# Kernel optimization log

Hardware: AMD Instinct MI355X
Metric: run time of the kernel (lower is better)

Reference implementation:

```python
import jax, jax.numpy as jnp
import numpy as np

B, N, C, H = 8, 1024, 1024, 16
HD = C // H
SCALE = HD ** -0.5


def setup_inputs() -> dict:
    key = jax.random.key(0)
    ks = jax.random.split(key, 6)
    s = 0.02
    return {
        "x": jax.random.normal(ks[0], (B, N, C), dtype=jnp.float32),
        "z_cls": jax.random.normal(ks[1], (B, 2 * C), dtype=jnp.float32),
        "Wqkv": jax.random.normal(ks[2], (C, 3 * C), dtype=jnp.float32) * s,
        "Wkv_cls": jax.random.normal(ks[3], (2 * C, 2 * C), dtype=jnp.float32) * s,
        "Wproj": jax.random.normal(ks[4], (C, C), dtype=jnp.float32) * s,
        "bproj": jax.random.normal(ks[5], (C,), dtype=jnp.float32) * s,
    }


def reference(x, z_cls, Wqkv, Wkv_cls, Wproj, bproj):
    # qkv projection: [B,N,3C] -> q,k,v each [B,H,N,HD]
    qkv = (x @ Wqkv).reshape(B, N, 3, H, HD).transpose(2, 0, 3, 1, 4)
    q, k, v = qkv[0], qkv[1], qkv[2]
    # cls k/v: [B,2C] -> [B,H,1,HD] each
    kv_cls = (z_cls @ Wkv_cls).reshape(B, 1, 2, H, HD).transpose(2, 0, 3, 1, 4)
    k_cls, v_cls = kv_cls[0], kv_cls[1]
    k = jnp.concatenate([k_cls, k], axis=2)  # [B,H,N+1,HD]
    v = jnp.concatenate([v_cls, v], axis=2)
    attn = jax.nn.softmax(jnp.einsum("bhnd,bhmd->bhnm", q, k) * SCALE, axis=-1)
    out = jnp.einsum("bhnm,bhmd->bhnd", attn, v)  # [B,H,N,HD]
    out = out.transpose(0, 2, 1, 3).reshape(B, N, C)
    return out @ Wproj + bproj
```

## Files before the change

kernel.cpp:

```cpp
#include <hip/hip_runtime.h>


typedef __attribute__((ext_vector_type(8))) short bf16x8;
typedef __attribute__((ext_vector_type(8))) unsigned short u16x8;
typedef __attribute__((ext_vector_type(4))) float f32x4;

#define SL2E 0.18033688011112042f

__device__ __forceinline__ unsigned short f2bf(float f) {
  unsigned int u = __builtin_bit_cast(unsigned int, f);
  return (unsigned short)((u + 0x7FFFu + ((u >> 16) & 1u)) >> 16);
}

__device__ __forceinline__ unsigned int cvt_pk_bf16(float lo, float hi) {
  unsigned int r;
  asm("v_cvt_pk_bf16_f32 %0, %1, %2" : "=v"(r) : "v"(lo), "v"(hi));
  return r;
}

template <typename T>
__device__ __forceinline__ void gll16(const T* g, void* l) {
  __builtin_amdgcn_global_load_lds(
      (__attribute__((address_space(1))) void*)(const_cast<T*>(g)),
      (__attribute__((address_space(3))) void*)l, 16, 0, 0);
}

__global__ __launch_bounds__(256) void cvt_f2b(const float* __restrict__ in,
                                               unsigned short* __restrict__ out, int n) {
  int i = (blockIdx.x * 256 + threadIdx.x) * 8;
  if (i >= n) return;
  const float4* p4 = (const float4*)(in + i);
  float4 a = p4[0], b = p4[1];
  u16x8 o;
  o[0] = f2bf(a.x); o[1] = f2bf(a.y); o[2] = f2bf(a.z); o[3] = f2bf(a.w);
  o[4] = f2bf(b.x); o[5] = f2bf(b.y); o[6] = f2bf(b.z); o[7] = f2bf(b.w);
  *(u16x8*)(out + i) = o;
}

__global__ __launch_bounds__(256) void transpose_f2b(const float* __restrict__ in,
                                                     unsigned short* __restrict__ out,
                                                     int R, int C) {
  __shared__ float tile[32][33];
  int c0 = blockIdx.x * 32, r0 = blockIdx.y * 32;
  int tx = threadIdx.x, ty = threadIdx.y;
#pragma unroll
  for (int j = 0; j < 32; j += 8)
    tile[ty + j][tx] = in[(size_t)(r0 + ty + j) * C + c0 + tx];
  __syncthreads();
#pragma unroll
  for (int j = 0; j < 32; j += 8)
    out[(size_t)(c0 + ty + j) * R + r0 + tx] = f2bf(tile[tx][ty + j]);
}

__global__ __launch_bounds__(256) void kvcls_gemm(const float* __restrict__ z,
                                                  const float* __restrict__ W,
                                                  float* __restrict__ accum) {
  int cc = blockIdx.x >> 5;
  int kc = blockIdx.x & 31;
  int c = cc * 256 + threadIdx.x;
  int k0 = kc * 64;
  float acc[8] = {0, 0, 0, 0, 0, 0, 0, 0};
  const float* wp = W + (size_t)k0 * 2048 + c;
  for (int k = 0; k < 64; ++k) {
    float wv = wp[(size_t)k * 2048];
#pragma unroll
    for (int b = 0; b < 8; ++b) acc[b] += z[b * 2048 + k0 + k] * wv;
  }
#pragma unroll
  for (int b = 0; b < 8; ++b) atomicAdd(&accum[b * 2048 + c], acc[b]);
}

__global__ __launch_bounds__(256) void kvcls_scatter(const float* __restrict__ accum,
                                                     unsigned short* __restrict__ kbuf,
                                                     unsigned short* __restrict__ vbuf) {
  int i = blockIdx.x * 256 + threadIdx.x;
  int b = i >> 11, c = i & 2047;
  int t = c >> 10, h = (c >> 6) & 15, d = c & 63;
  int bh = b * 16 + h;
  unsigned short v = f2bf(accum[i]);
  if (t == 0) kbuf[((size_t)bh * 1088 + 0) * 64 + d] = v;
  else        vbuf[((size_t)bh * 64 + d) * 1088 + 0] = v;
}

__global__ __launch_bounds__(256) void gemm_qkv(const unsigned short* __restrict__ A,
                                                const unsigned short* __restrict__ Bt,
                                                unsigned short* __restrict__ qb,
                                                unsigned short* __restrict__ kbuf,
                                                unsigned short* __restrict__ vbuf) {
  constexpr int K = 1024;
  __shared__ __attribute__((aligned(16))) unsigned short As[128 * 64];
  __shared__ __attribute__((aligned(16))) unsigned short Bs[128 * 64];
  int t = threadIdx.x, w = t >> 6, l = t & 63;
  int wg = (blockIdx.x & 7) * 192 + (blockIdx.x >> 3);
  int tm = wg / 24, tn = wg % 24;
  int m0 = tm * 128, n0 = tn * 128;
  int wr = w >> 1, wc = w & 1;
  int g = l >> 4, q = l & 15;
  f32x4 acc[4][4] = {};
  for (int kt = 0; kt < K / 64; ++kt) {
    int k0 = kt * 64;
#pragma unroll
    for (int i = 0; i < 4; ++i) {
      int f = i * 4096 + t * 16;
      int row = f >> 7, colb = (f & 127) ^ ((row & 7) << 4);
      gll16(A + (size_t)(m0 + row) * K + k0 + (colb >> 1), (char*)As + f);
    }
#pragma unroll
    for (int i = 0; i < 4; ++i) {
      int f = i * 4096 + t * 16;
      int row = f >> 7, colb = (f & 127) ^ ((row & 7) << 4);
      gll16(Bt + (size_t)(n0 + row) * K + k0 + (colb >> 1), (char*)Bs + f);
    }
    __syncthreads();
#pragma unroll
    for (int kk = 0; kk < 2; ++kk) {
      bf16x8 af[4], bf[4];
#pragma unroll
      for (int m = 0; m < 4; ++m) {
        int row = wr * 64 + m * 16 + q;
        int cb = (kk * 64 + g * 16) ^ ((row & 7) << 4);
        af[m] = *(const bf16x8*)((const char*)As + row * 128 + cb);
      }
#pragma unroll
      for (int n = 0; n < 4; ++n) {
        int row = wc * 64 + n * 16 + q;
        int cb = (kk * 64 + g * 16) ^ ((row & 7) << 4);
        bf[n] = *(const bf16x8*)((const char*)Bs + row * 128 + cb);
      }
      __builtin_amdgcn_s_setprio(1);
#pragma unroll
      for (int m = 0; m < 4; ++m)
#pragma unroll
        for (int n = 0; n < 4; ++n)
          acc[m][n] = __builtin_amdgcn_mfma_f32_16x16x32_bf16(af[m], bf[n], acc[m][n], 0, 0, 0);
      __builtin_amdgcn_s_setprio(0);
    }
    __syncthreads();
  }
  int tsel = n0 >> 10;
  int b = m0 >> 10;
  int nqb = m0 & 1023, ncb = n0 & 1023;
#pragma unroll
  for (int m = 0; m < 4; ++m)
#pragma unroll
    for (int n = 0; n < 4; ++n)
#pragma unroll
      for (int r = 0; r < 4; ++r) {
        int nq = nqb + wr * 64 + m * 16 + g * 4 + r;
        int col = ncb + wc * 64 + n * 16 + q;
        int h = col >> 6, d = col & 63;
        int bh = b * 16 + h;
        unsigned short val = f2bf(acc[m][n][r]);
        if (tsel == 0)      qb[((size_t)bh * 1024 + nq) * 64 + d] = val;
        else if (tsel == 1) kbuf[((size_t)bh * 1088 + 1 + nq) * 64 + d] = val;
        else                vbuf[((size_t)bh * 64 + d) * 1088 + 1 + nq] = val;
      }
}

__global__ __launch_bounds__(256) void attn_kernel(const unsigned short* __restrict__ qbuf,
                                                   const unsigned short* __restrict__ kbuf,
                                                   const unsigned short* __restrict__ vbuf,
                                                   unsigned short* __restrict__ ob) {
  __shared__ __attribute__((aligned(16))) unsigned short Ks[2][64 * 64];
  __shared__ __attribute__((aligned(16))) unsigned short Vs[2][64 * 64];
  __shared__ __attribute__((aligned(16))) unsigned short Ps[4][16 * 64];
  int t = threadIdx.x, w = t >> 6, l = t & 63;
  int g = l >> 4, q = l & 15;
  int wg = (blockIdx.x & 7) * 256 + (blockIdx.x >> 3);
  int bh = wg >> 4, qt = wg & 15;

  const unsigned short* qrow = qbuf + ((size_t)bh * 1024 + qt * 64 + w * 16 + q) * 64;
  bf16x8 qf[2];
  qf[0] = *(const bf16x8*)(qrow + g * 8);
  qf[1] = *(const bf16x8*)(qrow + 32 + g * 8);

  const unsigned short* kg = kbuf + (size_t)bh * 1088 * 64;
  const unsigned short* vg = vbuf + (size_t)bh * 64 * 1088;
  char* Pw = (char*)Ps[w];

  auto STAGE = [&](int bb, int kt) {
#pragma unroll
    for (int i = 0; i < 2; ++i) {
      int f = i * 4096 + t * 16;
      int row = f >> 7, colb = (f & 127) ^ ((row & 7) << 4);
      gll16(kg + (size_t)(kt * 64 + row) * 64 + (colb >> 1), (char*)Ks[bb] + f);
      gll16(vg + (size_t)row * 1088 + kt * 64 + (colb >> 1), (char*)Vs[bb] + f);
    }
  };

  STAGE(0, 0);
  __syncthreads();

  f32x4 o[4] = {};
  float mrun = -__builtin_inff(), lrun = 0.f;
  int swz = (q & 7) << 4;

  for (int kt = 0; kt < 17; ++kt) {
    int cur = kt & 1;
    if (kt < 16) STAGE(cur ^ 1, kt + 1);
    f32x4 s[4] = {};
#pragma unroll
    for (int kk = 0; kk < 2; ++kk) {
      bf16x8 kf[4];
#pragma unroll
      for (int n = 0; n < 4; ++n) {
        int cb = (kk * 64 + g * 16) ^ swz;
        kf[n] = *(const bf16x8*)((const char*)Ks[cur] + (n * 16 + q) * 128 + cb);
      }
      __builtin_amdgcn_s_setprio(1);
#pragma unroll
      for (int n = 0; n < 4; ++n)
        s[n] = __builtin_amdgcn_mfma_f32_16x16x32_bf16(kf[n], qf[kk], s[n], 0, 0, 0);
      __builtin_amdgcn_s_setprio(0);
    }
    if (kt == 16) {
#pragma unroll
      for (int n = 0; n < 4; ++n)
#pragma unroll
        for (int r = 0; r < 4; ++r)
          if (n | r) s[n][r] = -__builtin_inff();
      if (g != 0) s[0][0] = -__builtin_inff();
    }
    float mx = fmaxf(fmaxf(fmaxf(s[0][0], s[0][1]), fmaxf(s[0][2], s[0][3])),
                     fmaxf(fmaxf(s[1][0], s[1][1]), fmaxf(s[1][2], s[1][3])));
    mx = fmaxf(mx, fmaxf(fmaxf(fmaxf(s[2][0], s[2][1]), fmaxf(s[2][2], s[2][3])),
                         fmaxf(fmaxf(s[3][0], s[3][1]), fmaxf(s[3][2], s[3][3]))));
    mx = fmaxf(mx, __shfl_xor(mx, 16));
    mx = fmaxf(mx, __shfl_xor(mx, 32));
    float mnew;
    if (__all(mx <= mrun + 64.f)) {
      mnew = mrun;
    } else {
      mnew = fmaxf(mrun, mx);
      float fc = exp2f((mrun - mnew) * SL2E);
      mrun = mnew;
      lrun *= fc;
#pragma unroll
      for (int n = 0; n < 4; ++n) {
        o[n][0] *= fc; o[n][1] *= fc; o[n][2] *= fc; o[n][3] *= fc;
      }
    }
    float nb = mnew * SL2E;
    float rs = 0.f;
#pragma unroll
    for (int n = 0; n < 4; ++n)
#pragma unroll
      for (int r = 0; r < 4; ++r) {
        float p = exp2f(s[n][r] * SL2E - nb);
        s[n][r] = p;
        rs += p;
      }
    rs += __shfl_xor(rs, 16);
    rs += __shfl_xor(rs, 32);
    lrun += rs;
#pragma unroll
    for (int n = 0; n < 4; ++n) {
      uint2 pk;
      pk.x = cvt_pk_bf16(s[n][0], s[n][1]);
      pk.y = cvt_pk_bf16(s[n][2], s[n][3]);
      *(uint2*)(Pw + q * 128 + ((n * 32 + g * 8) ^ swz)) = pk;
    }
    asm volatile("s_waitcnt lgkmcnt(0)" ::: "memory");
#pragma unroll
    for (int kk = 0; kk < 2; ++kk) {
      bf16x8 pb = *(const bf16x8*)(Pw + q * 128 + ((kk * 64 + g * 16) ^ swz));
      bf16x8 vf[4];
#pragma unroll
      for (int n = 0; n < 4; ++n) {
        int cb = (kk * 64 + g * 16) ^ swz;
        vf[n] = *(const bf16x8*)((const char*)Vs[cur] + (n * 16 + q) * 128 + cb);
      }
      __builtin_amdgcn_s_setprio(1);
#pragma unroll
      for (int n = 0; n < 4; ++n)
        o[n] = __builtin_amdgcn_mfma_f32_16x16x32_bf16(vf[n], pb, o[n], 0, 0, 0);
      __builtin_amdgcn_s_setprio(0);
    }
    __syncthreads();
  }
  int b = bh >> 4, h = bh & 15;
  float inv = 1.0f / lrun;
  size_t rowg = (size_t)b * 1024 + qt * 64 + w * 16 + q;
#pragma unroll
  for (int n = 0; n < 4; ++n) {
    uint2 pk;
    pk.x = cvt_pk_bf16(o[n][0] * inv, o[n][1] * inv);
    pk.y = cvt_pk_bf16(o[n][2] * inv, o[n][3] * inv);
    *(uint2*)(ob + rowg * 1024 + h * 64 + n * 16 + g * 4) = pk;
  }
}

__global__ __launch_bounds__(256) void gemm_proj(const unsigned short* __restrict__ A,
                                                 const unsigned short* __restrict__ Bt,
                                                 const float* __restrict__ bias,
                                                 float* __restrict__ out) {
  constexpr int K = 1024;
  __shared__ __attribute__((aligned(16))) unsigned short As[128 * 64];
  __shared__ __attribute__((aligned(16))) unsigned short Bs[128 * 64];
  int t = threadIdx.x, w = t >> 6, l = t & 63;
  int wg = (blockIdx.x & 7) * 64 + (blockIdx.x >> 3);
  int tm = wg / 8, tn = wg % 8;
  int m0 = tm * 128, n0 = tn * 128;
  int wr = w >> 1, wc = w & 1;
  int g = l >> 4, q = l & 15;
  f32x4 acc[4][4] = {};
  for (int kt = 0; kt < K / 64; ++kt) {
    int k0 = kt * 64;
#pragma unroll
    for (int i = 0; i < 4; ++i) {
      int f = i * 4096 + t * 16;
      int row = f >> 7, colb = (f & 127) ^ ((row & 7) << 4);
      gll16(A + (size_t)(m0 + row) * K + k0 + (colb >> 1), (char*)As + f);
    }
#pragma unroll
    for (int i = 0; i < 4; ++i) {
      int f = i * 4096 + t * 16;
      int row = f >> 7, colb = (f & 127) ^ ((row & 7) << 4);
      gll16(Bt + (size_t)(n0 + row) * K + k0 + (colb >> 1), (char*)Bs + f);
    }
    __syncthreads();
#pragma unroll
    for (int kk = 0; kk < 2; ++kk) {
      bf16x8 af[4], bf[4];
#pragma unroll
      for (int m = 0; m < 4; ++m) {
        int row = wr * 64 + m * 16 + q;
        int cb = (kk * 64 + g * 16) ^ ((row & 7) << 4);
        af[m] = *(const bf16x8*)((const char*)As + row * 128 + cb);
      }
#pragma unroll
      for (int n = 0; n < 4; ++n) {
        int row = wc * 64 + n * 16 + q;
        int cb = (kk * 64 + g * 16) ^ ((row & 7) << 4);
        bf[n] = *(const bf16x8*)((const char*)Bs + row * 128 + cb);
      }
      __builtin_amdgcn_s_setprio(1);
#pragma unroll
      for (int m = 0; m < 4; ++m)
#pragma unroll
        for (int n = 0; n < 4; ++n)
          acc[m][n] = __builtin_amdgcn_mfma_f32_16x16x32_bf16(af[m], bf[n], acc[m][n], 0, 0, 0);
      __builtin_amdgcn_s_setprio(0);
    }
    __syncthreads();
  }
  float bv[4];
#pragma unroll
  for (int n = 0; n < 4; ++n) bv[n] = bias[n0 + wc * 64 + n * 16 + q];
#pragma unroll
  for (int m = 0; m < 4; ++m)
#pragma unroll
    for (int r = 0; r < 4; ++r) {
      size_t row = m0 + wr * 64 + m * 16 + g * 4 + r;
#pragma unroll
      for (int n = 0; n < 4; ++n) {
        int col = n0 + wc * 64 + n * 16 + q;
        out[row * 1024 + col] = acc[m][n][r] + bv[n];
      }
    }
}

extern "C" void kernel_launch(void* const* d_in, const int* in_sizes, int n_in,
                              void* d_out, int out_size, void* d_ws, size_t ws_size,
                              hipStream_t stream) {
  const float* x       = (const float*)d_in[0];
  const float* z_cls   = (const float*)d_in[1];
  const float* Wqkv    = (const float*)d_in[2];
  const float* Wkv_cls = (const float*)d_in[3];
  const float* Wproj   = (const float*)d_in[4];
  const float* bproj   = (const float*)d_in[5];
  float* out = (float*)d_out;

  char* p = (char*)d_ws;
  unsigned short* x_bf    = (unsigned short*)p; p += (size_t)8192 * 1024 * 2;
  unsigned short* wqkv_t  = (unsigned short*)p; p += (size_t)3072 * 1024 * 2;
  unsigned short* wproj_t = (unsigned short*)p; p += (size_t)1024 * 1024 * 2;
  unsigned short* q_buf   = (unsigned short*)p; p += (size_t)128 * 1024 * 64 * 2;
  unsigned short* k_buf   = (unsigned short*)p; p += (size_t)128 * 1088 * 64 * 2;
  unsigned short* v_buf   = (unsigned short*)p; p += (size_t)128 * 64 * 1088 * 2;
  unsigned short* attn_o  = (unsigned short*)p; p += (size_t)8192 * 1024 * 2;
  float* accum            = (float*)p;          p += (size_t)8 * 2048 * 4;

  hipMemsetAsync(accum, 0, 8 * 2048 * 4, stream);
  cvt_f2b<<<4096, 256, 0, stream>>>(x, x_bf, 8388608);
  transpose_f2b<<<dim3(96, 32), dim3(32, 8), 0, stream>>>(Wqkv, wqkv_t, 1024, 3072);
  transpose_f2b<<<dim3(32, 32), dim3(32, 8), 0, stream>>>(Wproj, wproj_t, 1024, 1024);
  kvcls_gemm<<<256, 256, 0, stream>>>(z_cls, Wkv_cls, accum);
  kvcls_scatter<<<64, 256, 0, stream>>>(accum, k_buf, v_buf);
  gemm_qkv<<<1536, 256, 0, stream>>>(x_bf, wqkv_t, q_buf, k_buf, v_buf);
  attn_kernel<<<2048, 256, 0, stream>>>(q_buf, k_buf, v_buf, attn_o);
  gemm_proj<<<512, 256, 0, stream>>>(attn_o, wproj_t, bproj, out);
}
```

Measured before the change: 319.3 us.

## Double-buffer QKV and projection GEMMs with larger 256-row tiles and 512 threads

Both GEMMs now use larger block tiles (256x256 for QKV, 256x128 for projection) with 8 waves per block. A double-buffered LDS pipeline prefetches the next K-slice via global_load_lds while the current one is consumed, synchronised with vmcnt waits and raw barriers. This aims to hide global-load latency and raise data reuse per LDS byte. In exchange it uses more LDS and registers per block, and on 256 CUs the grids of 384 and 256 blocks fill the machine less evenly.

```diff
diff --git a/kernel.cpp b/kernel.cpp
--- a/kernel.cpp
+++ b/kernel.cpp
@@ -82,71 +82,84 @@
   else        vbuf[((size_t)bh * 64 + d) * 1088 + 0] = v;
 }
 
-__global__ __launch_bounds__(256) void gemm_qkv(const unsigned short* __restrict__ A,
-                                                const unsigned short* __restrict__ Bt,
-                                                unsigned short* __restrict__ qb,
-                                                unsigned short* __restrict__ kbuf,
-                                                unsigned short* __restrict__ vbuf) {
-  constexpr int K = 1024;
-  __shared__ __attribute__((aligned(16))) unsigned short As[128 * 64];
-  __shared__ __attribute__((aligned(16))) unsigned short Bs[128 * 64];
+__global__ __launch_bounds__(512, 2) void gemm_qkv(const unsigned short* __restrict__ A,
+                                                   const unsigned short* __restrict__ Bt,
+                                                   unsigned short* __restrict__ qb,
+                                                   unsigned short* __restrict__ kbuf,
+                                                   unsigned short* __restrict__ vbuf) {
+  __shared__ __attribute__((aligned(16))) unsigned short As[2][256 * 64];
+  __shared__ __attribute__((aligned(16))) unsigned short Bs[2][256 * 64];
   int t = threadIdx.x, w = t >> 6, l = t & 63;
-  int wg = (blockIdx.x & 7) * 192 + (blockIdx.x >> 3);
-  int tm = wg / 24, tn = wg % 24;
-  int m0 = tm * 128, n0 = tn * 128;
-  int wr = w >> 1, wc = w & 1;
   int g = l >> 4, q = l & 15;
-  f32x4 acc[4][4] = {};
-  for (int kt = 0; kt < K / 64; ++kt) {
-    int k0 = kt * 64;
+  int wg = ((int)blockIdx.x & 7) * 48 + ((int)blockIdx.x >> 3);
+  int tm = wg / 12, tn = wg % 12;
+  int m0 = tm * 256, n0 = tn * 256;
+  int wr = w >> 2, wc = w & 3;
+
+  auto STAGE = [&](int bb, int k0) {
 #pragma unroll
     for (int i = 0; i < 4; ++i) {
-      int f = i * 4096 + t * 16;
+      int f = i * 8192 + t * 16;
       int row = f >> 7, colb = (f & 127) ^ ((row & 7) << 4);
-      gll16(A + (size_t)(m0 + row) * K + k0 + (colb >> 1), (char*)As + f);
+      gll16(A + (size_t)(m0 + row) * 1024 + k0 + (colb >> 1), (char*)As[bb] + f);
     }
 #pragma unroll
     for (int i = 0; i < 4; ++i) {
-      int f = i * 4096 + t * 16;
+      int f = i * 8192 + t * 16;
       int row = f >> 7, colb = (f & 127) ^ ((row & 7) << 4);
-      gll16(Bt + (size_t)(n0 + row) * K + k0 + (colb >> 1), (char*)Bs + f);
-    }
-    __syncthreads();
+      gll16(Bt + (size_t)(n0 + row) * 1024 + k0 + (colb >> 1), (char*)Bs[bb] + f);
+    }
+  };
+
+  f32x4 acc[8][4] = {};
+  STAGE(0, 0);
+  for (int kt = 0; kt < 16; ++kt) {
+    int cur = kt & 1;
+    if (kt < 15) {
+      STAGE(cur ^ 1, (kt + 1) * 64);
+      asm volatile("s_waitcnt vmcnt(8)" ::: "memory");
+    } else {
+      asm volatile("s_waitcnt vmcnt(0)" ::: "memory");
+    }
+    __builtin_amdgcn_s_barrier();
+    asm volatile("" ::: "memory");
+    const char* Ac = (const char*)As[cur];
+    const char* Bc = (const char*)Bs[cur];
 #pragma unroll
     for (int kk = 0; kk < 2; ++kk) {
-      bf16x8 af[4], bf[4];
-#pragma unroll
-      for (int m = 0; m < 4; ++m) {
-        int row = wr * 64 + m * 16 + q;
-        int cb = (kk * 64 + g * 16) ^ ((row & 7) << 4);
-        af[m] = *(const bf16x8*)((const char*)As + row * 128 + cb);
+      bf16x8 af[8], bf[4];
+#pragma unroll
+      for (int m = 0; m < 8; ++m) {
+        int row = wr * 128 + m * 16 + q;
+        af[m] = *(const bf16x8*)(Ac + row * 128 + ((kk * 64 + g * 16) ^ ((row & 7) << 4)));
       }
 #pragma unroll
       for (int n = 0; n < 4; ++n) {
         int row = wc * 64 + n * 16 + q;
-        int cb = (kk * 64 + g * 16) ^ ((row & 7) << 4);
-        bf[n] = *(const bf16x8*)((const char*)Bs + row * 128 + cb);
+        bf[n] = *(const bf16x8*)(Bc + row * 128 + ((kk * 64 + g * 16) ^ ((row & 7) << 4)));
       }
       __builtin_amdgcn_s_setprio(1);
 #pragma unroll
-      for (int m = 0; m < 4; ++m)
+      for (int m = 0; m < 8; ++m)
 #pragma unroll
         for (int n = 0; n < 4; ++n)
           acc[m][n] = __builtin_amdgcn_mfma_f32_16x16x32_bf16(af[m], bf[n], acc[m][n], 0, 0, 0);
       __builtin_amdgcn_s_setprio(0);
     }
-    __syncthreads();
+    asm volatile("" ::: "memory");
+    __builtin_amdgcn_s_barrier();
+    asm volatile("" ::: "memory");
   }
   int tsel = n0 >> 10;
   int b = m0 >> 10;
   int nqb = m0 & 1023, ncb = n0 & 1023;
 #pragma unroll
-  for (int m = 0; m < 4; ++m)
+  for (int m = 0; m < 8; ++m)
 #pragma unroll
     for (int n = 0; n < 4; ++n)
 #pragma unroll
       for (int r = 0; r < 4; ++r) {
-        int nq = nqb + wr * 64 + m * 16 + g * 4 + r;
+        int nq = nqb + wr * 128 + m * 16 + g * 4 + r;
         int col = ncb + wc * 64 + n * 16 + q;
         int h = col >> 6, d = col & 63;
         int bh = b * 16 + h;
@@ -290,71 +303,84 @@
   }
 }
 
-__global__ __launch_bounds__(256) void gemm_proj(const unsigned short* __restrict__ A,
-                                                 const unsigned short* __restrict__ Bt,
-                                                 const float* __restrict__ bias,
-                                                 float* __restrict__ out) {
-  constexpr int K = 1024;
-  __shared__ __attribute__((aligned(16))) unsigned short As[128 * 64];
-  __shared__ __attribute__((aligned(16))) unsigned short Bs[128 * 64];
+__global__ __launch_bounds__(512, 2) void gemm_proj(const unsigned short* __restrict__ A,
+                                                    const unsigned short* __restrict__ Bt,
+                                                    const float* __restrict__ bias,
+                                                    float* __restrict__ out) {
+  __shared__ __attribute__((aligned(16))) unsigned short As[2][256 * 64];
+  __shared__ __attribute__((aligned(16))) unsigned short Bs[2][128 * 64];
   int t = threadIdx.x, w = t >> 6, l = t & 63;
-  int wg = (blockIdx.x & 7) * 64 + (blockIdx.x >> 3);
+  int g = l >> 4, q = l & 15;
+  int wg = ((int)blockIdx.x & 7) * 32 + ((int)blockIdx.x >> 3);
   int tm = wg / 8, tn = wg % 8;
-  int m0 = tm * 128, n0 = tn * 128;
-  int wr = w >> 1, wc = w & 1;
-  int g = l >> 4, q = l & 15;
-  f32x4 acc[4][4] = {};
-  for (int kt = 0; kt < K / 64; ++kt) {
-    int k0 = kt * 64;
+  int m0 = tm * 256, n0 = tn * 128;
+  int wr = w >> 2, wc = w & 3;
+
+  auto STAGE = [&](int bb, int k0) {
 #pragma unroll
     for (int i = 0; i < 4; ++i) {
-      int f = i * 4096 + t * 16;
+      int f = i * 8192 + t * 16;
       int row = f >> 7, colb = (f & 127) ^ ((row & 7) << 4);
-      gll16(A + (size_t)(m0 + row) * K + k0 + (colb >> 1), (char*)As + f);
-    }
-#pragma unroll
-    for (int i = 0; i < 4; ++i) {
-      int f = i * 4096 + t * 16;
+      gll16(A + (size_t)(m0 + row) * 1024 + k0 + (colb >> 1), (char*)As[bb] + f);
+    }
+#pragma unroll
+    for (int i = 0; i < 2; ++i) {
+      int f = i * 8192 + t * 16;
       int row = f >> 7, colb = (f & 127) ^ ((row & 7) << 4);
-      gll16(Bt + (size_t)(n0 + row) * K + k0 + (colb >> 1), (char*)Bs + f);
-    }
-    __syncthreads();
+      gll16(Bt + (size_t)(n0 + row) * 1024 + k0 + (colb >> 1), (char*)Bs[bb] + f);
+    }
+  };
+
+  f32x4 acc[8][2] = {};
+  STAGE(0, 0);
+  for (int kt = 0; kt < 16; ++kt) {
+    int cur = kt & 1;
+    if (kt < 15) {
+      STAGE(cur ^ 1, (kt + 1) * 64);
+      asm volatile("s_waitcnt vmcnt(6)" ::: "memory");
+    } else {
+      asm volatile("s_waitcnt vmcnt(0)" ::: "memory");
+    }
+    __builtin_amdgcn_s_barrier();
+    asm volatile("" ::: "memory");
+    const char* Ac = (const char*)As[cur];
+    const char* Bc = (const char*)Bs[cur];
 #pragma unroll
     for (int kk = 0; kk < 2; ++kk) {
-      bf16x8 af[4], bf[4];
-#pragma unroll
-      for (int m = 0; m < 4; ++m) {
-        int row = wr * 64 + m * 16 + q;
-        int cb = (kk * 64 + g * 16) ^ ((row & 7) << 4);
-        af[m] = *(const bf16x8*)((const char*)As + row * 128 + cb);
-      }
-#pragma unroll
-      for (int n = 0; n < 4; ++n) {
-        int row = wc * 64 + n * 16 + q;
-        int cb = (kk * 64 + g * 16) ^ ((row & 7) << 4);
-        bf[n] = *(const bf16x8*)((const char*)Bs + row * 128 + cb);
+      bf16x8 af[8], bf[2];
+#pragma unroll
+      for (int m = 0; m < 8; ++m) {
+        int row = wr * 128 + m * 16 + q;
+        af[m] = *(const bf16x8*)(Ac + row * 128 + ((kk * 64 + g * 16) ^ ((row & 7) << 4)));
+      }
+#pragma unroll
+      for (int n = 0; n < 2; ++n) {
+        int row = wc * 32 + n * 16 + q;
+        bf[n] = *(const bf16x8*)(Bc + row * 128 + ((kk * 64 + g * 16) ^ ((row & 7) << 4)));
       }
       __builtin_amdgcn_s_setprio(1);
 #pragma unroll
-      for (int m = 0; m < 4; ++m)
-#pragma unroll
-        for (int n = 0; n < 4; ++n)
+      for (int m = 0; m < 8; ++m)
+#pragma unroll
+        for (int n = 0; n < 2; ++n)
           acc[m][n] = __builtin_amdgcn_mfma_f32_16x16x32_bf16(af[m], bf[n], acc[m][n], 0, 0, 0);
       __builtin_amdgcn_s_setprio(0);
     }
-    __syncthreads();
+    asm volatile("" ::: "memory");
+    __builtin_amdgcn_s_barrier();
+    asm volatile("" ::: "memory");
   }
-  float bv[4];
-#pragma unroll
-  for (int n = 0; n < 4; ++n) bv[n] = bias[n0 + wc * 64 + n * 16 + q];
-#pragma unroll
-  for (int m = 0; m < 4; ++m)
+  float bv[2];
+#pragma unroll
+  for (int n = 0; n < 2; ++n) bv[n] = bias[n0 + wc * 32 + n * 16 + q];
+#pragma unroll
+  for (int m = 0; m < 8; ++m)
 #pragma unroll
     for (int r = 0; r < 4; ++r) {
-      size_t row = m0 + wr * 64 + m * 16 + g * 4 + r;
-#pragma unroll
-      for (int n = 0; n < 4; ++n) {
-        int col = n0 + wc * 64 + n * 16 + q;
+      size_t row = m0 + wr * 128 + m * 16 + g * 4 + r;
+#pragma unroll
+      for (int n = 0; n < 2; ++n) {
+        int col = n0 + wc * 32 + n * 16 + q;
         out[row * 1024 + col] = acc[m][n][r] + bv[n];
       }
     }
@@ -387,7 +413,7 @@
   transpose_f2b<<<dim3(32, 32), dim3(32, 8), 0, stream>>>(Wproj, wproj_t, 1024, 1024);
   kvcls_gemm<<<256, 256, 0, stream>>>(z_cls, Wkv_cls, accum);
   kvcls_scatter<<<64, 256, 0, stream>>>(accum, k_buf, v_buf);
-  gemm_qkv<<<1536, 256, 0, stream>>>(x_bf, wqkv_t, q_buf, k_buf, v_buf);
+  gemm_qkv<<<384, 512, 0, stream>>>(x_bf, wqkv_t, q_buf, k_buf, v_buf);
   attn_kernel<<<2048, 256, 0, stream>>>(q_buf, k_buf, v_buf, attn_o);
-  gemm_proj<<<512, 256, 0, stream>>>(attn_o, wproj_t, bproj, out);
-}
+  gemm_proj<<<256, 512, 0, stream>>>(attn_o, wproj_t, bproj, out);
+}
```

After: 332.2 us. 4.0% more time.

## Use 256x256 double-buffered 8-wave GEMM tiles for QKV and projection

Applied to the files above, without the earlier changes.

Both GEMMs move from 128x128 tiles with 4 waves and single-buffered LDS to 256x256 tiles with 8 waves. The LDS buffers are now double-buffered, and the next K-slice is prefetched in the middle of the MFMA phases using explicit vmcnt waits and barriers. The aim is to hide global-load latency and raise arithmetic intensity per tile. In exchange it uses 128KB of LDS per block and more accumulator registers, and gemm_proj is left with only 128 blocks, which may underfill the GPU.

```diff
diff --git a/kernel.cpp b/kernel.cpp
--- a/kernel.cpp
+++ b/kernel.cpp
@@ -82,71 +82,94 @@
   else        vbuf[((size_t)bh * 64 + d) * 1088 + 0] = v;
 }
 
-__global__ __launch_bounds__(256) void gemm_qkv(const unsigned short* __restrict__ A,
-                                                const unsigned short* __restrict__ Bt,
-                                                unsigned short* __restrict__ qb,
-                                                unsigned short* __restrict__ kbuf,
-                                                unsigned short* __restrict__ vbuf) {
-  constexpr int K = 1024;
-  __shared__ __attribute__((aligned(16))) unsigned short As[128 * 64];
-  __shared__ __attribute__((aligned(16))) unsigned short Bs[128 * 64];
+#define GEMM256_LOOP(A_, B_, m0_, n0_)                                                 \
+  f32x4 acc[8][4] = {};                                                                \
+  auto STAGE_A = [&](int bb, int kt) {                                                 \
+    _Pragma("unroll") for (int h = 0; h < 2; ++h)                                      \
+    _Pragma("unroll") for (int i = 0; i < 2; ++i) {                                    \
+      int f = i * 8192 + t * 16;                                                       \
+      int row = f >> 7, colb = (f & 127) ^ ((row & 7) << 4);                           \
+      gll16(A_ + (size_t)(m0_ + h * 128 + row) * 1024 + kt * 64 + (colb >> 1),         \
+            (char*)As[bb][h] + f);                                                     \
+    }                                                                                  \
+  };                                                                                   \
+  auto STAGE_B = [&](int bb, int kt) {                                                 \
+    _Pragma("unroll") for (int h = 0; h < 2; ++h)                                      \
+    _Pragma("unroll") for (int i = 0; i < 2; ++i) {                                    \
+      int f = i * 8192 + t * 16;                                                       \
+      int row = f >> 7, colb = (f & 127) ^ ((row & 7) << 4);                           \
+      gll16(B_ + (size_t)(n0_ + h * 128 + row) * 1024 + kt * 64 + (colb >> 1),         \
+            (char*)Bs[bb][h] + f);                                                     \
+    }                                                                                  \
+  };                                                                                   \
+  STAGE_A(0, 0); STAGE_B(0, 0);                                                        \
+  STAGE_A(1, 1); STAGE_B(1, 1);                                                        \
+  asm volatile("s_waitcnt vmcnt(8)" ::: "memory");                                     \
+  __builtin_amdgcn_s_barrier();                                                        \
+  int brow_base = (wc & 1) * 64;                                                       \
+  for (int t16 = 0; t16 < 16; ++t16) {                                                 \
+    int c = t16 & 1;                                                                   \
+    const char* Ac = (const char*)As[c][wr];                                           \
+    const char* Bc = (const char*)Bs[c][wc >> 1];                                      \
+    bf16x8 bfr[4];                                                                     \
+    _Pragma("unroll") for (int p = 0; p < 4; ++p) {                                    \
+      int kk = p >> 1, mh = p & 1;                                                     \
+      bf16x8 afr[4];                                                                   \
+      if (mh == 0) {                                                                   \
+        _Pragma("unroll") for (int n = 0; n < 4; ++n) {                                \
+          int row = brow_base + n * 16 + q;                                            \
+          bfr[n] = *(const bf16x8*)(Bc + row * 128 +                                   \
+                                    ((kk * 64 + g * 16) ^ ((row & 7) << 4)));          \
+        }                                                                              \
+      }                                                                                \
+      _Pragma("unroll") for (int mi = 0; mi < 4; ++mi) {                               \
+        int row = mh * 64 + mi * 16 + q;                                               \
+        afr[mi] = *(const bf16x8*)(Ac + row * 128 +                                    \
+                                   ((kk * 64 + g * 16) ^ ((row & 7) << 4)));           \
+      }                                                                                \
+      if (p == 0 && t16 >= 1 && t16 <= 14) STAGE_A(c ^ 1, t16 + 1);                    \
+      if (p == 1 && t16 >= 1 && t16 <= 14) STAGE_B(c ^ 1, t16 + 1);                    \
+      __builtin_amdgcn_s_barrier();                                                    \
+      __builtin_amdgcn_sched_barrier(0);                                               \
+      __builtin_amdgcn_s_setprio(1);                                                   \
+      _Pragma("unroll") for (int mi = 0; mi < 4; ++mi)                                 \
+      _Pragma("unroll") for (int n = 0; n < 4; ++n)                                    \
+        acc[mh * 4 + mi][n] =                                                          \
+            __builtin_amdgcn_mfma_f32_16x16x32_bf16(afr[mi], bfr[n],                   \
+                                                    acc[mh * 4 + mi][n], 0, 0, 0);     \
+      __builtin_amdgcn_s_setprio(0);                                                   \
+      __builtin_amdgcn_sched_barrier(0);                                               \
+      if (p == 3 && t16 < 15) asm volatile("s_waitcnt vmcnt(0)" ::: "memory");         \
+      __builtin_amdgcn_s_barrier();                                                    \
+    }                                                                                  \
+  }
+
+__global__ __launch_bounds__(512, 2) void gemm_qkv(const unsigned short* __restrict__ A,
+                                                   const unsigned short* __restrict__ Bt,
+                                                   unsigned short* __restrict__ qb,
+                                                   unsigned short* __restrict__ kbuf,
+                                                   unsigned short* __restrict__ vbuf) {
+  __shared__ __attribute__((aligned(16))) unsigned short As[2][2][128 * 64];
+  __shared__ __attribute__((aligned(16))) unsigned short Bs[2][2][128 * 64];
   int t = threadIdx.x, w = t >> 6, l = t & 63;
-  int wg = (blockIdx.x & 7) * 192 + (blockIdx.x >> 3);
-  int tm = wg / 24, tn = wg % 24;
-  int m0 = tm * 128, n0 = tn * 128;
-  int wr = w >> 1, wc = w & 1;
   int g = l >> 4, q = l & 15;
-  f32x4 acc[4][4] = {};
-  for (int kt = 0; kt < K / 64; ++kt) {
-    int k0 = kt * 64;
-#pragma unroll
-    for (int i = 0; i < 4; ++i) {
-      int f = i * 4096 + t * 16;
-      int row = f >> 7, colb = (f & 127) ^ ((row & 7) << 4);
-      gll16(A + (size_t)(m0 + row) * K + k0 + (colb >> 1), (char*)As + f);
-    }
-#pragma unroll
-    for (int i = 0; i < 4; ++i) {
-      int f = i * 4096 + t * 16;
-      int row = f >> 7, colb = (f & 127) ^ ((row & 7) << 4);
-      gll16(Bt + (size_t)(n0 + row) * K + k0 + (colb >> 1), (char*)Bs + f);
-    }
-    __syncthreads();
-#pragma unroll
-    for (int kk = 0; kk < 2; ++kk) {
-      bf16x8 af[4], bf[4];
-#pragma unroll
-      for (int m = 0; m < 4; ++m) {
-        int row = wr * 64 + m * 16 + q;
-        int cb = (kk * 64 + g * 16) ^ ((row & 7) << 4);
-        af[m] = *(const bf16x8*)((const char*)As + row * 128 + cb);
-      }
-#pragma unroll
-      for (int n = 0; n < 4; ++n) {
-        int row = wc * 64 + n * 16 + q;
-        int cb = (kk * 64 + g * 16) ^ ((row & 7) << 4);
-        bf[n] = *(const bf16x8*)((const char*)Bs + row * 128 + cb);
-      }
-      __builtin_amdgcn_s_setprio(1);
-#pragma unroll
-      for (int m = 0; m < 4; ++m)
-#pragma unroll
-        for (int n = 0; n < 4; ++n)
-          acc[m][n] = __builtin_amdgcn_mfma_f32_16x16x32_bf16(af[m], bf[n], acc[m][n], 0, 0, 0);
-      __builtin_amdgcn_s_setprio(0);
-    }
-    __syncthreads();
-  }
+  int wg = ((int)blockIdx.x & 7) * 48 + ((int)blockIdx.x >> 3);
+  int tm = wg / 12, tn = wg % 12;
+  int m0 = tm * 256, n0 = tn * 256;
+  int wr = w >> 2, wc = w & 3;
+
+  GEMM256_LOOP(A, Bt, m0, n0)
+
   int tsel = n0 >> 10;
   int b = m0 >> 10;
   int nqb = m0 & 1023, ncb = n0 & 1023;
 #pragma unroll
-  for (int m = 0; m < 4; ++m)
+  for (int m = 0; m < 8; ++m)
 #pragma unroll
     for (int n = 0; n < 4; ++n)
 #pragma unroll
       for (int r = 0; r < 4; ++r) {
-        int nq = nqb + wr * 64 + m * 16 + g * 4 + r;
+        int nq = nqb + wr * 128 + m * 16 + g * 4 + r;
         int col = ncb + wc * 64 + n * 16 + q;
         int h = col >> 6, d = col & 63;
         int bh = b * 16 + h;
@@ -155,6 +178,37 @@
         else if (tsel == 1) kbuf[((size_t)bh * 1088 + 1 + nq) * 64 + d] = val;
         else                vbuf[((size_t)bh * 64 + d) * 1088 + 1 + nq] = val;
       }
+}
+
+__global__ __launch_bounds__(512, 2) void gemm_proj(const unsigned short* __restrict__ A,
+                                                    const unsigned short* __restrict__ Bt,
+                                                    const float* __restrict__ bias,
+                                                    float* __restrict__ out) {
+  __shared__ __attribute__((aligned(16))) unsigned short As[2][2][128 * 64];
+  __shared__ __attribute__((aligned(16))) unsigned short Bs[2][2][128 * 64];
+  int t = threadIdx.x, w = t >> 6, l = t & 63;
+  int g = l >> 4, q = l & 15;
+  int wg = ((int)blockIdx.x & 7) * 16 + ((int)blockIdx.x >> 3);
+  int tm = wg / 4, tn = wg % 4;
+  int m0 = tm * 256, n0 = tn * 256;
+  int wr = w >> 2, wc = w & 3;
+
+  GEMM256_LOOP(A, Bt, m0, n0)
+
+  float bv[4];
+#pragma unroll
+  for (int n = 0; n < 4; ++n) bv[n] = bias[n0 + wc * 64 + n * 16 + q];
+#pragma unroll
+  for (int m = 0; m < 8; ++m)
+#pragma unroll
+    for (int r = 0; r < 4; ++r) {
+      size_t row = m0 + wr * 128 + m * 16 + g * 4 + r;
+#pragma unroll
+      for (int n = 0; n < 4; ++n) {
+        int col = n0 + wc * 64 + n * 16 + q;
+        out[row * 1024 + col] = acc[m][n][r] + bv[n];
+      }
+    }
 }
 
 __global__ __launch_bounds__(256) void attn_kernel(const unsigned short* __restrict__ qbuf,
@@ -290,76 +344,6 @@
   }
 }
 
-__global__ __launch_bounds__(256) void gemm_proj(const unsigned short* __restrict__ A,
-                                                 const unsigned short* __restrict__ Bt,
-                                                 const float* __restrict__ bias,
-                                                 float* __restrict__ out) {
-  constexpr int K = 1024;
-  __shared__ __attribute__((aligned(16))) unsigned short As[128 * 64];
-  __shared__ __attribute__((aligned(16))) unsigned short Bs[128 * 64];
-  int t = threadIdx.x, w = t >> 6, l = t & 63;
-  int wg = (blockIdx.x & 7) * 64 + (blockIdx.x >> 3);
-  int tm = wg / 8, tn = wg % 8;
-  int m0 = tm * 128, n0 = tn * 128;
-  int wr = w >> 1, wc = w & 1;
-  int g = l >> 4, q = l & 15;
-  f32x4 acc[4][4] = {};
-  for (int kt = 0; kt < K / 64; ++kt) {
-    int k0 = kt * 64;
-#pragma unroll
-    for (int i = 0; i < 4; ++i) {
-      int f = i * 4096 + t * 16;
-      int row = f >> 7, colb = (f & 127) ^ ((row & 7) << 4);
-      gll16(A + (size_t)(m0 + row) * K + k0 + (colb >> 1), (char*)As + f);
-    }
-#pragma unroll
-    for (int i = 0; i < 4; ++i) {
-      int f = i * 4096 + t * 16;
-      int row = f >> 7, colb = (f & 127) ^ ((row & 7) << 4);
-      gll16(Bt + (size_t)(n0 + row) * K + k0 + (colb >> 1), (char*)Bs + f);
-    }
-    __syncthreads();
-#pragma unroll
-    for (int kk = 0; kk < 2; ++kk) {
-      bf16x8 af[4], bf[4];
-#pragma unroll
-      for (int m = 0; m < 4; ++m) {
-        int row = wr * 64 + m * 16 + q;
-        int cb = (kk * 64 + g * 16) ^ ((row & 7) << 4);
-        af[m] = *(const bf16x8*)((const char*)As + row * 128 + cb);
-      }
-#pragma unroll
-      for (int n = 0; n < 4; ++n) {
-        int row = wc * 64 + n * 16 + q;
-        int cb = (kk * 64 + g * 16) ^ ((row & 7) << 4);
-        bf[n] = *(const bf16x8*)((const char*)Bs + row * 128 + cb);
-      }
-      __builtin_amdgcn_s_setprio(1);
-#pragma unroll
-      for (int m = 0; m < 4; ++m)
-#pragma unroll
-        for (int n = 0; n < 4; ++n)
-          acc[m][n] = __builtin_amdgcn_mfma_f32_16x16x32_bf16(af[m], bf[n], acc[m][n], 0, 0, 0);
-      __builtin_amdgcn_s_setprio(0);
-    }
-    __syncthreads();
-  }
-  float bv[4];
-#pragma unroll
-  for (int n = 0; n < 4; ++n) bv[n] = bias[n0 + wc * 64 + n * 16 + q];
-#pragma unroll
-  for (int m = 0; m < 4; ++m)
-#pragma unroll
-    for (int r = 0; r < 4; ++r) {
-      size_t row = m0 + wr * 64 + m * 16 + g * 4 + r;
-#pragma unroll
-      for (int n = 0; n < 4; ++n) {
-        int col = n0 + wc * 64 + n * 16 + q;
-        out[row * 1024 + col] = acc[m][n][r] + bv[n];
-      }
-    }
-}
-
 extern "C" void kernel_launch(void* const* d_in, const int* in_sizes, int n_in,
                               void* d_out, int out_size, void* d_ws, size_t ws_size,
                               hipStream_t stream) {
@@ -387,7 +371,7 @@
   transpose_f2b<<<dim3(32, 32), dim3(32, 8), 0, stream>>>(Wproj, wproj_t, 1024, 1024);
   kvcls_gemm<<<256, 256, 0, stream>>>(z_cls, Wkv_cls, accum);
   kvcls_scatter<<<64, 256, 0, stream>>>(accum, k_buf, v_buf);
-  gemm_qkv<<<1536, 256, 0, stream>>>(x_bf, wqkv_t, q_buf, k_buf, v_buf);
+  gemm_qkv<<<384, 512, 0, stream>>>(x_bf, wqkv_t, q_buf, k_buf, v_buf);
   attn_kernel<<<2048, 256, 0, stream>>>(q_buf, k_buf, v_buf, attn_o);
-  gemm_proj<<<512, 256, 0, stream>>>(attn_o, wproj_t, bproj, out);
-}
+  gemm_proj<<<128, 512, 0, stream>>>(attn_o, wproj_t, bproj, out);
+}
```

New measurement: 338.2 us. 1.06x slower.
